# Performance work log

Hardware: AMD Instinct MI355X
Metric: run time of the kernel (lower is better)

The kernel has to match this reference:

```python
import jax, jax.numpy as jnp
import numpy as np

DIM = 512
DIM2 = 2 * DIM
HEADS = 8
HEAD_DIM = DIM2 // HEADS
NB = 4                      # BlockDiagonalLinear blocks
BLK = DIM2 // NB
KS = 4                      # causal conv kernel size
EPS = 1e-5


def setup_inputs() -> dict:
    key = jax.random.key(0)
    ks = jax.random.split(key, 32)
    r = lambda i, shape, s=0.02: jax.random.normal(ks[i], shape, dtype=jnp.float32) * s
    inp = {
        "x": jax.random.normal(ks[0], (2, 2048, DIM), dtype=jnp.float32),
        "ln_w": jnp.ones((DIM,), jnp.float32),
        "ln_b": jnp.zeros((DIM,), jnp.float32),
        "mlp1_w": r(1, (DIM, DIM2)), "mlp1_b": jnp.zeros((DIM2,), jnp.float32),
        "mlp2_w": r(2, (DIM, DIM2)), "mlp2_b": jnp.zeros((DIM2,), jnp.float32),
        "conv_w": r(3, (DIM2, DIM2, KS)), "conv_b": jnp.zeros((DIM2,), jnp.float32),
        "bq_w": r(4, (NB, BLK, BLK)), "bk_w": r(5, (NB, BLK, BLK)), "bv_w": r(6, (NB, BLK, BLK)),
        "wq_w": r(7, (DIM2, DIM2)), "wq_b": jnp.zeros((DIM2,), jnp.float32),
        "wk_w": r(8, (DIM2, DIM2)), "wk_b": jnp.zeros((DIM2,), jnp.float32),
        "wv_w": r(9, (DIM2, DIM2)), "wv_b": jnp.zeros((DIM2,), jnp.float32),
        "wi_w": r(10, (DIM2, HEADS)), "wi_b": jnp.zeros((HEADS,), jnp.float32),
        "wf_w": r(11, (DIM2, HEADS)), "wf_b": jnp.zeros((HEADS,), jnp.float32),
        "gn_w": jnp.ones((DIM2,), jnp.float32), "gn_b": jnp.zeros((DIM2,), jnp.float32),
        "skip": jnp.ones((DIM2,), jnp.float32),
        "fin_w": r(12, (DIM2, DIM)), "fin_b": jnp.zeros((DIM,), jnp.float32),
    }
    return inp


def _layernorm(x, w, b):
    mu = jnp.mean(x, -1, keepdims=True)
    var = jnp.var(x, -1, keepdims=True)
    return (x - mu) * jax.lax.rsqrt(var + EPS) * w + b


def _block_linear(x, w):  # x: [b,s,DIM2], w: [NB, BLK, BLK]
    b, s, _ = x.shape
    xg = x.reshape(b, s, NB, BLK)
    return jnp.einsum('bsgi,gio->bsgo', xg, w).reshape(b, s, DIM2)


def _mlstm_cell(q, k, v, wq_w, wq_b, wk_w, wk_b, wv_w, wv_b,
                wi_w, wi_b, wf_w, wf_b, gn_w, gn_b):
    b, s, _ = q.shape
    tau = DIM2 ** 0.5
    itilde = jnp.einsum('bsd,dh->bhs', q, wi_w) + wi_b[None, :, None]   # [b,h,s]
    ftilde = jnp.einsum('bsd,dh->bhs', k, wf_w) + wf_b[None, :, None]   # [b,h,s]
    # cumulative log forget gates; F_act[i,j] = cs[i] - cs[j] on lower triangle
    cs = jnp.cumsum(jax.nn.log_sigmoid(ftilde), axis=-1)                # [b,h,s]
    mask = jnp.tril(jnp.ones((s, s), bool))
    Dtilde = jnp.where(mask,
                       cs[..., :, None] - cs[..., None, :] + itilde[..., None, :],
                       -jnp.inf)                                        # [b,h,s,s]
    max_d = jnp.max(Dtilde, axis=-1, keepdims=True)
    D = jnp.exp(Dtilde - max_d)
    qh = (q @ wq_w + wq_b).reshape(b, s, HEADS, HEAD_DIM).transpose(0, 2, 1, 3)
    kh = (k @ wk_w + wk_b).reshape(b, s, HEADS, HEAD_DIM).transpose(0, 2, 1, 3)
    vh = (v @ wv_w + wv_b).reshape(b, s, HEADS, HEAD_DIM).transpose(0, 2, 1, 3)
    Ctilde = jnp.einsum('bhid,bhjd->bhij', qh, kh) * D / tau
    maxit = jnp.maximum(jnp.abs(Ctilde.sum(-1)), jnp.exp(-max_d[..., 0]))  # [b,h,s]
    H = jnp.einsum('bhij,bhjd->bhid', Ctilde, vh) / (maxit[..., None] + 1e-8)
    H = H.transpose(0, 2, 1, 3)                                          # [b,s,h,hd]
    # GroupNorm(heads, DIM2): per (b,s,head-group) normalization
    mu = jnp.mean(H, -1, keepdims=True)
    var = jnp.var(H, -1, keepdims=True)
    Hn = (H - mu) * jax.lax.rsqrt(var + EPS)
    Hn = Hn * gn_w.reshape(HEADS, HEAD_DIM) + gn_b.reshape(HEADS, HEAD_DIM)
    return Hn.reshape(b, s, DIM2)


def reference(x, ln_w, ln_b, mlp1_w, mlp1_b, mlp2_w, mlp2_b, conv_w, conv_b,
              bq_w, bk_w, bv_w, wq_w, wq_b, wk_w, wk_b, wv_w, wv_b,
              wi_w, wi_b, wf_w, wf_b, gn_w, gn_b, skip, fin_w, fin_b):
    inputs = _layernorm(x, ln_w, ln_b)
    a = inputs @ mlp1_w + mlp1_b                 # [b,s,DIM2]
    bgate = jax.nn.silu(inputs @ mlp2_w + mlp2_b)
    # causal conv1d (left pad KS-1)
    ac = a.transpose(0, 2, 1)                    # [b,DIM2,s]
    qk = jax.lax.conv_general_dilated(ac, conv_w, (1,), [(KS - 1, 0)],
                                      dimension_numbers=('NCH', 'OIH', 'NCH'))
    qk = (qk + conv_b[None, :, None]).transpose(0, 2, 1)
    qk = jax.nn.silu(qk)
    q = _block_linear(qk, bq_w)
    k = _block_linear(qk, bk_w)
    v = _block_linear(a, bv_w)
    out1 = _mlstm_cell(q, k, v, wq_w, wq_b, wk_w, wk_b, wv_w, wv_b,
                       wi_w, wi_b, wf_w, wf_b, gn_w, gn_b)
    out1 = out1 + skip * qk
    out1 = out1 * bgate
    out1 = out1 @ fin_w + fin_b
    return x + out1
```

## Files before the change

kernel.cpp:

```cpp
#include <hip/hip_runtime.h>
#include <hip/hip_bf16.h>
#include <cmath>

typedef __hip_bfloat16 bf16;
typedef __attribute__((ext_vector_type(8))) short short8;
typedef __attribute__((ext_vector_type(4))) float f32x4;

#define SEQ   2048
#define DIMX  512
#define DIM2X 1024
#define NHEADS 8
#define HDIM  128
#define EPSF  1e-5f
#define PADROWS 2051

__device__ __forceinline__ float b2f(bf16 v) { return __bfloat162float(v); }
__device__ __forceinline__ bf16 f2b(float f) { return __float2bfloat16(f); }
__device__ __forceinline__ unsigned short f2bu(float f) { bf16 t = __float2bfloat16(f); return *(unsigned short*)&t; }

__device__ __forceinline__ void gl16(const bf16* g, bf16* l) {
  __builtin_amdgcn_global_load_lds((const __attribute__((address_space(1))) void*)g,
                                   (__attribute__((address_space(3))) void*)l, 16, 0, 0);
}

__global__ void __launch_bounds__(256) k_layernorm(const float* __restrict__ x,
                                                   const float* __restrict__ w,
                                                   const float* __restrict__ b,
                                                   bf16* __restrict__ out) {
  int row  = blockIdx.x * 4 + (threadIdx.x >> 6);
  int lane = threadIdx.x & 63;
  const float* xr = x + (size_t)row * DIMX;
  float v[8]; float s = 0.f, sq = 0.f;
#pragma unroll
  for (int i = 0; i < 8; i++) {
    float f = xr[lane + i * 64];
    v[i] = f; s += f; sq += f * f;
  }
#pragma unroll
  for (int off = 32; off; off >>= 1) { s += __shfl_xor(s, off); sq += __shfl_xor(sq, off); }
  float mu  = s * (1.f / DIMX);
  float var = sq * (1.f / DIMX) - mu * mu;
  float rs  = rsqrtf(var + EPSF);
  bf16* o = out + (size_t)row * DIMX;
#pragma unroll
  for (int i = 0; i < 8; i++) {
    int c = lane + i * 64;
    o[c] = f2b((v[i] - mu) * rs * w[c] + b[c]);
  }
}

__global__ void __launch_bounds__(256) k_castT3(const float* __restrict__ W0,
                                                const float* __restrict__ W1,
                                                const float* __restrict__ W2,
                                                bf16* __restrict__ WT,
                                                int K, int N, int innerZ, int gW, int gT) {
  __shared__ float t[32][33];
  const int z = blockIdx.z;
  const int sel = z / innerZ, zz = z % innerZ;
  const float* W = (sel == 0 ? W0 : sel == 1 ? W1 : W2) + (size_t)zz * gW;
  bf16* T = WT + (size_t)(sel * innerZ + zz) * gT;
  const int k0 = blockIdx.y * 32, n0 = blockIdx.x * 32;
  const int r = threadIdx.x >> 5, c = threadIdx.x & 31;
#pragma unroll
  for (int i = 0; i < 4; i++)
    t[r + i * 8][c] = W[(size_t)(k0 + r + i * 8) * N + n0 + c];
  __syncthreads();
#pragma unroll
  for (int i = 0; i < 4; i++)
    T[(size_t)(n0 + r + i * 8) * K + k0 + c] = f2b(t[c][r + i * 8]);
}

__global__ void __launch_bounds__(256) k_convwT(const float* __restrict__ cw, bf16* __restrict__ wc) {
  int idx = blockIdx.x * 256 + threadIdx.x;
  int o = idx >> 12, z = idx & 4095, kk = z >> 10, i = z & 1023;
  wc[idx] = f2b(cw[(size_t)o * 4096 + i * 4 + kk]);
}

__global__ void __launch_bounds__(256) k_zeropad(bf16* __restrict__ p) {
  int idx = blockIdx.x * 256 + threadIdx.x;
  int b = idx / 3072, off = idx % 3072;
  p[(size_t)b * PADROWS * DIM2X + off] = f2b(0.f);
}

__device__ __forceinline__ void mgemm_body(const bf16* A, int lda, const bf16* WT,
                                           const float* bias, void* Cv, const float* xres,
                                           int ldc, int K, int ACT, int STORE, int APAD,
                                           size_t coff, int bm, int bn) {
  __shared__ __align__(16) bf16 smA[4][128 * 32];
  __shared__ __align__(16) bf16 smB[4][64 * 32];
  const int tid  = threadIdx.x;
  const int lane = tid & 63;
  const int w = tid >> 6, wy = w >> 1, wx = w & 1;
  const int col = lane & 15, quad = lane >> 4;

  const int r4 = tid >> 2, c8 = (tid & 3) * 8;
  int ra0 = bm + r4, ra1 = bm + 64 + r4;
  if (APAD) { ra0 += (ra0 >> 11) * 3 + 3; ra1 += (ra1 >> 11) * 3 + 3; }
  const bf16* gA0 = A + (size_t)ra0 * lda + c8;
  const bf16* gA1 = A + (size_t)ra1 * lda + c8;
  const bf16* gB0 = WT + (size_t)(bn + r4) * K + c8;

  f32x4 acc[4][2];
#pragma unroll
  for (int a = 0; a < 4; a++)
#pragma unroll
    for (int b = 0; b < 2; b++) acc[a][b] = (f32x4){0.f, 0.f, 0.f, 0.f};

  const int laoff = (wy * 64) * 32, lboff = (wx * 32) * 32;
  const int lsa = r4 * 32 + c8;
  const int nsteps = K >> 5;

#define GSTAGE(buf, k0s)                                                       \
  do {                                                                         \
    gl16(gA0 + (k0s), &smA[buf][lsa]);                                         \
    gl16(gA1 + (k0s), &smA[buf][64 * 32 + lsa]);                               \
    gl16(gB0 + (k0s), &smB[buf][lsa]);                                         \
  } while (0)

  GSTAGE(0, 0);
  if (nsteps > 1) GSTAGE(1, 32);
  for (int s = 0; s < nsteps; ++s) {
    if (s + 2 < nsteps) GSTAGE((s + 2) & 3, (s + 2) * 32);
    if (s + 2 < nsteps)      asm volatile("s_waitcnt vmcnt(6)" ::: "memory");
    else if (s + 1 < nsteps) asm volatile("s_waitcnt vmcnt(3)" ::: "memory");
    else                     asm volatile("s_waitcnt vmcnt(0)" ::: "memory");
    __builtin_amdgcn_s_barrier();
    asm volatile("" ::: "memory");
    const bf16* bA = smA[s & 3];
    const bf16* bB = smB[s & 3];
    short8 af[4], bfr[2];
#pragma unroll
    for (int mt = 0; mt < 4; mt++)
      af[mt] = *(const short8*)&bA[laoff + (mt * 16 + col) * 32 + quad * 8];
#pragma unroll
    for (int nt = 0; nt < 2; nt++)
      bfr[nt] = *(const short8*)&bB[lboff + (nt * 16 + col) * 32 + quad * 8];
#pragma unroll
    for (int mt = 0; mt < 4; mt++)
#pragma unroll
      for (int nt = 0; nt < 2; nt++)
        acc[mt][nt] = __builtin_amdgcn_mfma_f32_16x16x32_bf16(af[mt], bfr[nt], acc[mt][nt], 0, 0, 0);
  }
#undef GSTAGE

#pragma unroll
  for (int mt = 0; mt < 4; mt++) {
#pragma unroll
    for (int nt = 0; nt < 2; nt++) {
      const int n = bn + wx * 32 + nt * 16 + col;
      const int mrow0 = bm + wy * 64 + mt * 16 + quad * 4;
      float bs = bias ? bias[n] : 0.f;
      if (STORE == 1) {
        bf16* C = (bf16*)Cv + coff;
        ushort4 pk;
        pk.x = f2bu(acc[mt][nt][0] + bs); pk.y = f2bu(acc[mt][nt][1] + bs);
        pk.z = f2bu(acc[mt][nt][2] + bs); pk.w = f2bu(acc[mt][nt][3] + bs);
        *(ushort4*)(C + (size_t)n * 4096 + mrow0) = pk;
      } else if (STORE == 2) {
        float* O = (float*)Cv + coff;
#pragma unroll
        for (int r = 0; r < 4; r++) {
          size_t gi = (size_t)(mrow0 + r) * ldc + n;
          O[gi] = acc[mt][nt][r] + bs + xres[gi];
        }
      } else if (STORE == 3) {
        bf16* C = (bf16*)Cv;
        const int pr = (mrow0 >> 11) * 3 + 3;
#pragma unroll
        for (int r = 0; r < 4; r++)
          C[(size_t)(mrow0 + pr + r) * ldc + n] = f2b(acc[mt][nt][r] + bs);
      } else {
        bf16* C = (bf16*)Cv + coff;
#pragma unroll
        for (int r = 0; r < 4; r++) {
          float v = acc[mt][nt][r] + bs;
          if (ACT == 1) v = v / (1.f + expf(-v));
          C[(size_t)(mrow0 + r) * ldc + n] = f2b(v);
        }
      }
    }
  }
}

__device__ __forceinline__ int xcd_work_id() {
  const int nx = gridDim.x, ny = gridDim.y;
  const int d = blockIdx.x + nx * (blockIdx.y + ny * blockIdx.z);
  const int q = (nx * ny * (int)gridDim.z) >> 3;
  return (d & 7) * q + (d >> 3);
}

template <int ACT, int STORE, int APAD>
__global__ void __launch_bounds__(256) k_mgemm(const bf16* __restrict__ A, int lda,
                                               const bf16* __restrict__ WT,
                                               const float* __restrict__ bias,
                                               void* __restrict__ Cv,
                                               const float* __restrict__ xres,
                                               int ldc, int K,
                                               int gA, int gW, int gC) {
  const int wk = xcd_work_id();
  const int nx = gridDim.x, ny = gridDim.y;
  const int wx = wk % nx, rest = wk / nx;
  const int wy = rest % ny, g = rest / ny;
  mgemm_body(A + (size_t)g * gA, lda, WT + (size_t)g * gW, bias, Cv, xres,
             ldc, K, ACT, STORE, APAD, (size_t)g * gC, wy * 128, wx * 64);
}

__global__ void __launch_bounds__(256) k_mgemmB(const bf16* A0, const bf16* A1, const bf16* A2,
                                                const bf16* W0, const bf16* W1, const bf16* W2,
                                                const float* b0, const float* b1, const float* b2,
                                                void* C0, void* C1, void* C2,
                                                int lda, int ldc, int K, int zPer,
                                                int gA, int gW, int gC,
                                                int actm, int storem, int apadm) {
  const int wk = xcd_work_id();
  const int nx = gridDim.x, ny = gridDim.y;
  const int wx = wk % nx, rest = wk / nx;
  const int wy = rest % ny, z = rest / ny;
  const int sel = z / zPer, zz = z % zPer;
  const bf16* A = (sel == 0 ? A0 : sel == 1 ? A1 : A2) + (size_t)zz * gA;
  const bf16* W = (sel == 0 ? W0 : sel == 1 ? W1 : W2) + (size_t)zz * gW;
  const float* bias = sel == 0 ? b0 : sel == 1 ? b1 : b2;
  void* Cv = sel == 0 ? C0 : sel == 1 ? C1 : C2;
  mgemm_body(A, lda, W, bias, Cv, nullptr, ldc, K,
             (actm >> sel) & 1, (storem >> (4 * sel)) & 15, (apadm >> sel) & 1,
             (size_t)zz * gC, wy * 128, wx * 64);
}

__global__ void __launch_bounds__(256) k_gates(const bf16* __restrict__ q, const bf16* __restrict__ kk,
                                               const float* __restrict__ wi, const float* __restrict__ wib,
                                               const float* __restrict__ wf, const float* __restrict__ wfb,
                                               float* __restrict__ it, float* __restrict__ ft) {
  int gid  = blockIdx.x * 4 + (threadIdx.x >> 6);
  int lane = threadIdx.x & 63;
  int which = gid >> 12;
  int m = gid & 4095;
  const bf16* row = (which ? kk : q) + (size_t)m * DIM2X;
  const float* w = which ? wf : wi;
  float s[8] = {0, 0, 0, 0, 0, 0, 0, 0};
  for (int d = lane; d < DIM2X; d += 64) {
    float xv = b2f(row[d]);
    const float4* wp = (const float4*)(w + d * 8);
    float4 w0 = wp[0], w1 = wp[1];
    s[0] += xv * w0.x; s[1] += xv * w0.y; s[2] += xv * w0.z; s[3] += xv * w0.w;
    s[4] += xv * w1.x; s[5] += xv * w1.y; s[6] += xv * w1.z; s[7] += xv * w1.w;
  }
#pragma unroll
  for (int off = 32; off; off >>= 1) {
#pragma unroll
    for (int h = 0; h < 8; h++) s[h] += __shfl_xor(s[h], off);
  }
  if (lane == 0) {
    int b_ = m >> 11, tt = m & 2047;
    const float* wb = which ? wfb : wib;
    float* dst = which ? ft : it;
#pragma unroll
    for (int h = 0; h < 8; h++)
      dst[((size_t)(b_ * NHEADS + h)) * SEQ + tt] = s[h] + wb[h];
  }
}

__global__ void __launch_bounds__(256) k_scan(const float* __restrict__ it, const float* __restrict__ ft,
                                              float* __restrict__ cs, float* __restrict__ md) {
  const int bh = blockIdx.x;
  const int t  = threadIdx.x;
  const float* fr = ft + (size_t)bh * SEQ;
  const float* ir = it + (size_t)bh * SEQ;
  float* csr = cs + (size_t)bh * SEQ;
  float* mdr = md + (size_t)bh * SEQ;
  __shared__ float tmp[256];
  float loc[8]; float run = 0.f;
#pragma unroll
  for (int j = 0; j < 8; j++) {
    float xv = fr[t * 8 + j];
    float ls = fminf(xv, 0.f) - log1pf(expf(-fabsf(xv)));
    run += ls; loc[j] = run;
  }
  tmp[t] = run;
  __syncthreads();
  for (int off = 1; off < 256; off <<= 1) {
    float add = (t >= off) ? tmp[t - off] : 0.f;
    __syncthreads();
    tmp[t] += add;
    __syncthreads();
  }
  float exc = (t == 0) ? 0.f : tmp[t - 1];
  float csv[8];
#pragma unroll
  for (int j = 0; j < 8; j++) { csv[j] = loc[j] + exc; csr[t * 8 + j] = csv[j]; }
  __syncthreads();
  float rmax = -INFINITY; float gm[8];
#pragma unroll
  for (int j = 0; j < 8; j++) {
    float gv = ir[t * 8 + j] - csv[j];
    rmax = fmaxf(rmax, gv); gm[j] = rmax;
  }
  tmp[t] = rmax;
  __syncthreads();
  for (int off = 1; off < 256; off <<= 1) {
    float other = (t >= off) ? tmp[t - off] : -INFINITY;
    __syncthreads();
    tmp[t] = fmaxf(tmp[t], other);
    __syncthreads();
  }
  float emax = (t == 0) ? -INFINITY : tmp[t - 1];
#pragma unroll
  for (int j = 0; j < 8; j++) mdr[t * 8 + j] = csv[j] + fmaxf(gm[j], emax);
}

__global__ void __launch_bounds__(256) k_attn_mfma(const bf16* __restrict__ qh,
                                                   const bf16* __restrict__ kh,
                                                   const bf16* __restrict__ vt,
                                                   const float* __restrict__ cs,
                                                   const float* __restrict__ md,
                                                   const float* __restrict__ itl,
                                                   bf16* __restrict__ Hout) {
  const int bh = blockIdx.y, b_ = bh >> 3, h = bh & 7;
  const int pr = blockIdx.x;
  const int tid = threadIdx.x;
  const int w = tid >> 6;
  const int lane = tid & 63;
  const int col = lane & 15, quad = lane >> 4;
  const float L2E = 1.44269504f;

  __shared__ __align__(16) bf16 smK[4 * 4096];
  __shared__ __align__(16) bf16 smV[4 * 4096];
  __shared__ __align__(16) bf16 Sc[4][16][40];

  const size_t baseQK = ((size_t)b_ * SEQ) * DIM2X + (size_t)h * HDIM;
  const size_t vtb = (size_t)(h * HDIM) * 4096 + (size_t)b_ * SEQ;
  const float* csp = cs + (size_t)bh * SEQ;
  const float* mdp = md + (size_t)bh * SEQ;
  const float* itp = itl + (size_t)bh * SEQ;

  const int kj = tid >> 4, kq = tid & 15;
  const bf16* gKs = kh + baseQK + (size_t)kj * DIM2X + ((kq ^ (kj & 7)) * 8);
  const int vn = tid >> 2, vq = tid & 3;
  const bf16* gVs = vt + vtb + (size_t)vn * 4096 + ((vq ^ ((vn >> 1) & 3)) * 8);

#define STAGE(buf, j0s)                                                        \
  do {                                                                         \
    bf16* dK = &smK[(buf) * 4096 + tid * 8];                                   \
    gl16(gKs + (size_t)(j0s) * DIM2X, dK);                                     \
    gl16(gKs + (size_t)((j0s) + 16) * DIM2X, dK + 2048);                       \
    bf16* dV = &smV[(buf) * 4096 + tid * 8];                                   \
    gl16(gVs + (j0s), dV);                                                     \
    gl16(gVs + (j0s) + (size_t)64 * 4096, dV + 2048);                          \
  } while (0)

  for (int ph = 0; ph < 2; ++ph) {
    const int tile = ph ? (31 - pr) : pr;
    const int i0 = tile * 64;
    const int i0w = i0 + w * 16;
    const int iwmax = i0w + 15;

    short8 qf[4];
#pragma unroll
    for (int kc = 0; kc < 4; kc++)
      qf[kc] = *(const short8*)(qh + baseQK + (size_t)(i0w + col) * DIM2X + kc * 32 + quad * 8);

    float cs_i[4], md_i[4];
#pragma unroll
    for (int r = 0; r < 4; r++) {
      int i = i0w + quad * 4 + r;
      cs_i[r] = csp[i] * L2E; md_i[r] = mdp[i] * L2E;
    }

    f32x4 accpv[8];
#pragma unroll
    for (int nb = 0; nb < 8; nb++) accpv[nb] = (f32x4){0.f, 0.f, 0.f, 0.f};
    float rs[4] = {0.f, 0.f, 0.f, 0.f};

    const int trips = 2 * tile + 2;
    STAGE(0, 0);
    STAGE(1, 32);
    for (int t = 0; t < trips; ++t) {
      const int cur = t & 3;
      const int j0p = t * 32;
      if (t + 2 < trips) STAGE((t + 2) & 3, j0p + 64);
      if (t + 2 < trips)      asm volatile("s_waitcnt vmcnt(8)" ::: "memory");
      else if (t + 1 < trips) asm volatile("s_waitcnt vmcnt(4)" ::: "memory");
      else                    asm volatile("s_waitcnt vmcnt(0)" ::: "memory");
      __builtin_amdgcn_s_barrier();
      asm volatile("" ::: "memory");
      if (j0p <= iwmax) {
        float g0 = (itp[j0p + col] - csp[j0p + col]) * L2E;
        float g1 = (itp[j0p + 16 + col] - csp[j0p + 16 + col]) * L2E;
        const bool jt1 = (j0p + 16 <= iwmax);
#pragma unroll
        for (int jt = 0; jt < 2; jt++) {
          const int j0 = j0p + jt * 16;
          float sv[4] = {0.f, 0.f, 0.f, 0.f};
          if (jt == 0 || jt1) {
            const int jj = jt * 16 + col;
            f32x4 aq = (f32x4){0.f, 0.f, 0.f, 0.f};
#pragma unroll
            for (int kc = 0; kc < 4; kc++) {
              short8 bk = *(const short8*)&smK[cur * 4096 + jj * 128 + ((((kc << 2) | quad) ^ (jj & 7)) << 3)];
              aq = __builtin_amdgcn_mfma_f32_16x16x32_bf16(qf[kc], bk, aq, 0, 0, 0);
            }
            const int j = j0 + col;
            const float gj = jt ? g1 : g0;
#pragma unroll
            for (int r = 0; r < 4; r++) {
              const int i = i0w + quad * 4 + r;
              float s = (j <= i) ? exp2f(cs_i[r] + gj - md_i[r] - 5.f) * aq[r] : 0.f;
              sv[r] = s; rs[r] += s;
            }
          }
#pragma unroll
          for (int r = 0; r < 4; r++) Sc[w][quad * 4 + r][jt * 16 + col] = f2b(sv[r]);
        }
        asm volatile("s_waitcnt lgkmcnt(0)" ::: "memory");
        __builtin_amdgcn_sched_barrier(0);
        short8 af = *(const short8*)(&Sc[w][col][quad * 8]);
#pragma unroll
        for (int nb = 0; nb < 8; nb++) {
          const int rn = nb * 16 + col;
          short8 bv = *(const short8*)&smV[cur * 4096 + rn * 32 + ((quad ^ ((rn >> 1) & 3)) << 3)];
          accpv[nb] = __builtin_amdgcn_mfma_f32_16x16x32_bf16(af, bv, accpv[nb], 0, 0, 0);
        }
      }
    }
    __syncthreads();

#pragma unroll
    for (int r = 0; r < 4; r++) {
      float v = rs[r];
      v += __shfl_xor(v, 1); v += __shfl_xor(v, 2);
      v += __shfl_xor(v, 4); v += __shfl_xor(v, 8);
      rs[r] = v;
    }
    float inv[4];
#pragma unroll
    for (int r = 0; r < 4; r++) {
      float maxit = fmaxf(fabsf(rs[r]), exp2f(fminf(-md_i[r], 43.f)));
      inv[r] = 1.f / (maxit + 1e-8f);
    }
#pragma unroll
    for (int nb = 0; nb < 8; nb++)
#pragma unroll
      for (int r = 0; r < 4; r++)
        Hout[baseQK + (size_t)(i0w + quad * 4 + r) * DIM2X + nb * 16 + col] = f2b(accpv[nb][r] * inv[r]);
  }
#undef STAGE
}

__global__ void __launch_bounds__(256) k_gnorm(const bf16* __restrict__ H, const bf16* __restrict__ qk,
                                               const bf16* __restrict__ bg,
                                               const float* __restrict__ gw, const float* __restrict__ gb,
                                               const float* __restrict__ skip, bf16* __restrict__ pre) {
  int gid  = blockIdx.x * 4 + (threadIdx.x >> 6);
  int lane = threadIdx.x & 63;
  int m = gid >> 3, h = gid & 7;
  const bf16* Hr = H + (size_t)m * DIM2X + (size_t)h * HDIM;
  float v0 = b2f(Hr[lane]), v1 = b2f(Hr[lane + 64]);
  float s = v0 + v1, sq = v0 * v0 + v1 * v1;
#pragma unroll
  for (int off = 32; off; off >>= 1) { s += __shfl_xor(s, off); sq += __shfl_xor(sq, off); }
  float mu  = s * (1.f / 128.f);
  float var = sq * (1.f / 128.f) - mu * mu;
  float rs  = rsqrtf(var + EPSF);
#pragma unroll
  for (int e = 0; e < 2; e++) {
    int c = lane + e * 64;
    int col = h * HDIM + c;
    float v = e ? v1 : v0;
    float hn = (v - mu) * rs * gw[col] + gb[col];
    size_t gidx = (size_t)m * DIM2X + col;
    pre[gidx] = f2b((hn + skip[col] * b2f(qk[gidx])) * b2f(bg[gidx]));
  }
}

extern "C" void kernel_launch(void* const* d_in, const int* in_sizes, int n_in,
                              void* d_out, int out_size, void* d_ws, size_t ws_size,
                              hipStream_t stream) {
  const float* x     = (const float*)d_in[0];
  const float* ln_w  = (const float*)d_in[1];
  const float* ln_b  = (const float*)d_in[2];
  const float* mlp1w = (const float*)d_in[3];
  const float* mlp1b = (const float*)d_in[4];
  const float* mlp2w = (const float*)d_in[5];
  const float* mlp2b = (const float*)d_in[6];
  const float* convw = (const float*)d_in[7];
  const float* convb = (const float*)d_in[8];
  const float* bqw   = (const float*)d_in[9];
  const float* bkw   = (const float*)d_in[10];
  const float* bvw   = (const float*)d_in[11];
  const float* wqw   = (const float*)d_in[12];
  const float* wqb   = (const float*)d_in[13];
  const float* wkw   = (const float*)d_in[14];
  const float* wkb   = (const float*)d_in[15];
  const float* wvw   = (const float*)d_in[16];
  const float* wvb   = (const float*)d_in[17];
  const float* wiw   = (const float*)d_in[18];
  const float* wib   = (const float*)d_in[19];
  const float* wfw   = (const float*)d_in[20];
  const float* wfb   = (const float*)d_in[21];
  const float* gnw   = (const float*)d_in[22];
  const float* gnb   = (const float*)d_in[23];
  const float* skip  = (const float*)d_in[24];
  const float* finw  = (const float*)d_in[25];
  const float* finb  = (const float*)d_in[26];
  float* out = (float*)d_out;

  float* GA  = (float*)d_ws;
  float* ITb = GA;
  float* FTb = GA + 32768;
  float* CSb = GA + 65536;
  float* MDb = GA + 98304;
  const size_t SLOT = 4u * 1024u * 1024u;
  bf16* S0 = (bf16*)((char*)d_ws + (1 << 20));
  bf16* S1 = S0 + SLOT;
  bf16* S2 = S1 + SLOT;
  bf16* S3 = S2 + SLOT;
  bf16* S4 = S3 + SLOT;
  bf16* S5 = S4 + SLOT;
  bf16* S6 = S5 + SLOT;
  bf16 *LN = S0, *BG = S2, *QKb = S3, *Qb = S4, *Kb = S5, *Vb = S6;
  bf16 *QH = S0, *KH = S1, *VT = S4, *Hb = S5, *PRE = S6;
  bf16* WTb   = S6 + SLOT;
  bf16* mlp1T = WTb;
  bf16* mlp2T = WTb + 524288;
  bf16* convT = WTb + 1048576;
  bf16* bqT   = WTb + 5242880;
  bf16* bkT   = bqT + 262144;
  bf16* bvT   = bkT + 262144;
  bf16* wqT   = bvT + 262144;
  bf16* wkT   = wqT + 1048576;
  bf16* wvT   = wkT + 1048576;
  bf16* finT  = wvT + 1048576;
  bf16* APD   = finT + 524288;

  k_castT3<<<dim3(32, 16, 2), 256, 0, stream>>>(mlp1w, mlp2w, mlp2w, mlp1T, DIMX, DIM2X, 1, 0, 524288);
  k_castT3<<<dim3(32, 32, 3), 256, 0, stream>>>(wqw, wkw, wvw, wqT, DIM2X, DIM2X, 1, 0, 1048576);
  k_castT3<<<dim3(8, 8, 12), 256, 0, stream>>>(bqw, bkw, bvw, bqT, 256, 256, 4, 65536, 65536);
  k_castT3<<<dim3(16, 32, 1), 256, 0, stream>>>(finw, finw, finw, finT, DIM2X, DIMX, 1, 0, 524288);
  k_convwT<<<16384, 256, 0, stream>>>(convw, convT);
  k_zeropad<<<24, 256, 0, stream>>>(APD);

  k_layernorm<<<1024, 256, 0, stream>>>(x, ln_w, ln_b, LN);
  k_mgemmB<<<dim3(16, 32, 2), 256, 0, stream>>>(LN, LN, LN, mlp1T, mlp2T, mlp2T,
                                                mlp1b, mlp2b, mlp2b, APD, BG, BG,
                                                DIMX, DIM2X, DIMX, 1, 0, 0, 0,
                                                 0b10,  3 | (0 << 4),  0);
  k_mgemm<1, 0, 0><<<dim3(16, 16, 2), 256, 0, stream>>>(APD, DIM2X, convT, convb, QKb, nullptr,
                                                        DIM2X, 4096, PADROWS * DIM2X, 0, SEQ * DIM2X);
  k_mgemmB<<<dim3(4, 32, 12), 256, 0, stream>>>(QKb, QKb, APD, bqT, bkT, bvT,
                                                nullptr, nullptr, nullptr, Qb, Kb, Vb,
                                                DIM2X, DIM2X, 256, 4, 256, 65536, 256,
                                                 0,  0,  0b100);
  k_gates<<<2048, 256, 0, stream>>>(Qb, Kb, wiw, wib, wfw, wfb, ITb, FTb);
  k_scan<<<16, 256, 0, stream>>>(ITb, FTb, CSb, MDb);
  k_mgemmB<<<dim3(16, 32, 3), 256, 0, stream>>>(Qb, Kb, Vb, wqT, wkT, wvT,
                                                wqb, wkb, wvb, QH, KH, VT,
                                                DIM2X, DIM2X, DIM2X, 1, 0, 0, 0,
                                                 0,  0 | (0 << 4) | (1 << 8),  0);
  k_attn_mfma<<<dim3(16, 16), 256, 0, stream>>>(QH, KH, VT, CSb, MDb, ITb, Hb);
  k_gnorm<<<8192, 256, 0, stream>>>(Hb, QKb, BG, gnw, gnb, skip, PRE);
  k_mgemm<0, 2, 0><<<dim3(8, 32), 256, 0, stream>>>(PRE, DIM2X, finT, finb, out, x, DIMX, DIM2X, 0, 0, 0);
}
```

Measured before the change: 460.5 us.

## Fuse group-norm/skip/gate epilogue into attention kernel and split tile pairs into blocks

The per-head group norm, skip connection and output gate move into the attention kernel's epilogue, using in-register accumulators with shuffle reductions across the 128 head columns. This removes the separate gnorm kernel and the bf16 H buffer round-trip. The attention grid is also doubled so each block processes one query tile rather than a paired short/long tile, with ordering alternated by batch. This raises parallelism but may worsen causal load balance.

```diff
diff --git a/kernel.cpp b/kernel.cpp
--- a/kernel.cpp
+++ b/kernel.cpp
@@ -313,13 +313,22 @@
                                                    const float* __restrict__ cs,
                                                    const float* __restrict__ md,
                                                    const float* __restrict__ itl,
-                                                   bf16* __restrict__ Hout) {
+                                                   const bf16* __restrict__ qk,
+                                                   const bf16* __restrict__ bg,
+                                                   const float* __restrict__ gw,
+                                                   const float* __restrict__ gb,
+                                                   const float* __restrict__ skip,
+                                                   bf16* __restrict__ pre) {
   const int bh = blockIdx.y, b_ = bh >> 3, h = bh & 7;
-  const int pr = blockIdx.x;
+  const int bx = blockIdx.x;
+  const int tile = ((blockIdx.y >> 3) & 1) ? bx : 31 - bx;
+  const int i0 = tile * 64;
   const int tid = threadIdx.x;
   const int w = tid >> 6;
   const int lane = tid & 63;
   const int col = lane & 15, quad = lane >> 4;
+  const int i0w = i0 + w * 16;
+  const int iwmax = i0w + 15;
   const float L2E = 1.44269504f;
 
   __shared__ __align__(16) bf16 smK[4 * 4096];
@@ -332,10 +341,29 @@
   const float* mdp = md + (size_t)bh * SEQ;
   const float* itp = itl + (size_t)bh * SEQ;
 
+  short8 qf[4];
+#pragma unroll
+  for (int kc = 0; kc < 4; kc++)
+    qf[kc] = *(const short8*)(qh + baseQK + (size_t)(i0w + col) * DIM2X + kc * 32 + quad * 8);
+
+  float cs_i[4], md_i[4];
+#pragma unroll
+  for (int r = 0; r < 4; r++) {
+    int i = i0w + quad * 4 + r;
+    cs_i[r] = csp[i] * L2E; md_i[r] = mdp[i] * L2E;
+  }
+
+  f32x4 accpv[8];
+#pragma unroll
+  for (int nb = 0; nb < 8; nb++) accpv[nb] = (f32x4){0.f, 0.f, 0.f, 0.f};
+  float rs[4] = {0.f, 0.f, 0.f, 0.f};
+
   const int kj = tid >> 4, kq = tid & 15;
   const bf16* gKs = kh + baseQK + (size_t)kj * DIM2X + ((kq ^ (kj & 7)) * 8);
   const int vn = tid >> 2, vq = tid & 3;
   const bf16* gVs = vt + vtb + (size_t)vn * 4096 + ((vq ^ ((vn >> 1) & 3)) * 8);
+
+  const int trips = 2 * tile + 2;
 
 #define STAGE(buf, j0s)                                                        \
   do {                                                                         \
@@ -347,127 +375,101 @@
     gl16(gVs + (j0s) + (size_t)64 * 4096, dV + 2048);                          \
   } while (0)
 
-  for (int ph = 0; ph < 2; ++ph) {
-    const int tile = ph ? (31 - pr) : pr;
-    const int i0 = tile * 64;
-    const int i0w = i0 + w * 16;
-    const int iwmax = i0w + 15;
-
-    short8 qf[4];
-#pragma unroll
-    for (int kc = 0; kc < 4; kc++)
-      qf[kc] = *(const short8*)(qh + baseQK + (size_t)(i0w + col) * DIM2X + kc * 32 + quad * 8);
-
-    float cs_i[4], md_i[4];
-#pragma unroll
-    for (int r = 0; r < 4; r++) {
-      int i = i0w + quad * 4 + r;
-      cs_i[r] = csp[i] * L2E; md_i[r] = mdp[i] * L2E;
-    }
-
-    f32x4 accpv[8];
-#pragma unroll
-    for (int nb = 0; nb < 8; nb++) accpv[nb] = (f32x4){0.f, 0.f, 0.f, 0.f};
-    float rs[4] = {0.f, 0.f, 0.f, 0.f};
-
-    const int trips = 2 * tile + 2;
-    STAGE(0, 0);
-    STAGE(1, 32);
-    for (int t = 0; t < trips; ++t) {
-      const int cur = t & 3;
-      const int j0p = t * 32;
-      if (t + 2 < trips) STAGE((t + 2) & 3, j0p + 64);
-      if (t + 2 < trips)      asm volatile("s_waitcnt vmcnt(8)" ::: "memory");
-      else if (t + 1 < trips) asm volatile("s_waitcnt vmcnt(4)" ::: "memory");
-      else                    asm volatile("s_waitcnt vmcnt(0)" ::: "memory");
-      __builtin_amdgcn_s_barrier();
-      asm volatile("" ::: "memory");
-      if (j0p <= iwmax) {
-        float g0 = (itp[j0p + col] - csp[j0p + col]) * L2E;
-        float g1 = (itp[j0p + 16 + col] - csp[j0p + 16 + col]) * L2E;
-        const bool jt1 = (j0p + 16 <= iwmax);
-#pragma unroll
-        for (int jt = 0; jt < 2; jt++) {
-          const int j0 = j0p + jt * 16;
-          float sv[4] = {0.f, 0.f, 0.f, 0.f};
-          if (jt == 0 || jt1) {
-            const int jj = jt * 16 + col;
-            f32x4 aq = (f32x4){0.f, 0.f, 0.f, 0.f};
-#pragma unroll
-            for (int kc = 0; kc < 4; kc++) {
-              short8 bk = *(const short8*)&smK[cur * 4096 + jj * 128 + ((((kc << 2) | quad) ^ (jj & 7)) << 3)];
-              aq = __builtin_amdgcn_mfma_f32_16x16x32_bf16(qf[kc], bk, aq, 0, 0, 0);
-            }
-            const int j = j0 + col;
-            const float gj = jt ? g1 : g0;
-#pragma unroll
-            for (int r = 0; r < 4; r++) {
-              const int i = i0w + quad * 4 + r;
-              float s = (j <= i) ? exp2f(cs_i[r] + gj - md_i[r] - 5.f) * aq[r] : 0.f;
-              sv[r] = s; rs[r] += s;
-            }
+  STAGE(0, 0);
+  STAGE(1, 32);
+  for (int t = 0; t < trips; ++t) {
+    const int cur = t & 3;
+    const int j0p = t * 32;
+    if (t + 2 < trips) STAGE((t + 2) & 3, j0p + 64);
+    if (t + 2 < trips)      asm volatile("s_waitcnt vmcnt(8)" ::: "memory");
+    else if (t + 1 < trips) asm volatile("s_waitcnt vmcnt(4)" ::: "memory");
+    else                    asm volatile("s_waitcnt vmcnt(0)" ::: "memory");
+    __builtin_amdgcn_s_barrier();
+    asm volatile("" ::: "memory");
+    if (j0p <= iwmax) {
+      float g0 = (itp[j0p + col] - csp[j0p + col]) * L2E;
+      float g1 = (itp[j0p + 16 + col] - csp[j0p + 16 + col]) * L2E;
+      const bool jt1 = (j0p + 16 <= iwmax);
+#pragma unroll
+      for (int jt = 0; jt < 2; jt++) {
+        const int j0 = j0p + jt * 16;
+        float sv[4] = {0.f, 0.f, 0.f, 0.f};
+        if (jt == 0 || jt1) {
+          const int jj = jt * 16 + col;
+          f32x4 aq = (f32x4){0.f, 0.f, 0.f, 0.f};
+#pragma unroll
+          for (int kc = 0; kc < 4; kc++) {
+            short8 bk = *(const short8*)&smK[cur * 4096 + jj * 128 + ((((kc << 2) | quad) ^ (jj & 7)) << 3)];
+            aq = __builtin_amdgcn_mfma_f32_16x16x32_bf16(qf[kc], bk, aq, 0, 0, 0);
           }
-#pragma unroll
-          for (int r = 0; r < 4; r++) Sc[w][quad * 4 + r][jt * 16 + col] = f2b(sv[r]);
+          const int j = j0 + col;
+          const float gj = jt ? g1 : g0;
+#pragma unroll
+          for (int r = 0; r < 4; r++) {
+            const int i = i0w + quad * 4 + r;
+            float s = (j <= i) ? exp2f(cs_i[r] + gj - md_i[r] - 5.f) * aq[r] : 0.f;
+            sv[r] = s; rs[r] += s;
+          }
         }
-        asm volatile("s_waitcnt lgkmcnt(0)" ::: "memory");
-        __builtin_amdgcn_sched_barrier(0);
-        short8 af = *(const short8*)(&Sc[w][col][quad * 8]);
-#pragma unroll
-        for (int nb = 0; nb < 8; nb++) {
-          const int rn = nb * 16 + col;
-          short8 bv = *(const short8*)&smV[cur * 4096 + rn * 32 + ((quad ^ ((rn >> 1) & 3)) << 3)];
-          accpv[nb] = __builtin_amdgcn_mfma_f32_16x16x32_bf16(af, bv, accpv[nb], 0, 0, 0);
-        }
+#pragma unroll
+        for (int r = 0; r < 4; r++) Sc[w][quad * 4 + r][jt * 16 + col] = f2b(sv[r]);
+      }
+      asm volatile("s_waitcnt lgkmcnt(0)" ::: "memory");
+      __builtin_amdgcn_sched_barrier(0);
+      short8 af = *(const short8*)(&Sc[w][col][quad * 8]);
+#pragma unroll
+      for (int nb = 0; nb < 8; nb++) {
+        const int rn = nb * 16 + col;
+        short8 bv = *(const short8*)&smV[cur * 4096 + rn * 32 + ((quad ^ ((rn >> 1) & 3)) << 3)];
+        accpv[nb] = __builtin_amdgcn_mfma_f32_16x16x32_bf16(af, bv, accpv[nb], 0, 0, 0);
       }
     }
-    __syncthreads();
-
-#pragma unroll
-    for (int r = 0; r < 4; r++) {
-      float v = rs[r];
-      v += __shfl_xor(v, 1); v += __shfl_xor(v, 2);
-      v += __shfl_xor(v, 4); v += __shfl_xor(v, 8);
-      rs[r] = v;
+  }
+#undef STAGE
+
+#pragma unroll
+  for (int r = 0; r < 4; r++) {
+    float v = rs[r];
+    v += __shfl_xor(v, 1); v += __shfl_xor(v, 2);
+    v += __shfl_xor(v, 4); v += __shfl_xor(v, 8);
+    rs[r] = v;
+  }
+  float inv[4];
+#pragma unroll
+  for (int r = 0; r < 4; r++) {
+    float maxit = fmaxf(fabsf(rs[r]), exp2f(fminf(-md_i[r], 43.f)));
+    inv[r] = 1.f / (maxit + 1e-8f);
+  }
+  float gwv[8], gbv[8], skv[8];
+#pragma unroll
+  for (int nb = 0; nb < 8; nb++) {
+    int c = h * HDIM + nb * 16 + col;
+    gwv[nb] = gw[c]; gbv[nb] = gb[c]; skv[nb] = skip[c];
+  }
+#pragma unroll
+  for (int r = 0; r < 4; r++) {
+    const int row = i0w + quad * 4 + r;
+    float s1 = 0.f, s2 = 0.f;
+#pragma unroll
+    for (int nb = 0; nb < 8; nb++) {
+      float v = accpv[nb][r] * inv[r];
+      s1 += v; s2 += v * v;
     }
-    float inv[4];
-#pragma unroll
-    for (int r = 0; r < 4; r++) {
-      float maxit = fmaxf(fabsf(rs[r]), exp2f(fminf(-md_i[r], 43.f)));
-      inv[r] = 1.f / (maxit + 1e-8f);
+    s1 += __shfl_xor(s1, 1); s2 += __shfl_xor(s2, 1);
+    s1 += __shfl_xor(s1, 2); s2 += __shfl_xor(s2, 2);
+    s1 += __shfl_xor(s1, 4); s2 += __shfl_xor(s2, 4);
+    s1 += __shfl_xor(s1, 8); s2 += __shfl_xor(s2, 8);
+    float mu  = s1 * (1.f / 128.f);
+    float var = s2 * (1.f / 128.f) - mu * mu;
+    float rsg = rsqrtf(var + EPSF);
+    const size_t rbase = baseQK + (size_t)row * DIM2X;
+#pragma unroll
+    for (int nb = 0; nb < 8; nb++) {
+      float hv = accpv[nb][r] * inv[r];
+      float hn = (hv - mu) * rsg * gwv[nb] + gbv[nb];
+      size_t gi = rbase + nb * 16 + col;
+      pre[gi] = f2b((hn + skv[nb] * b2f(qk[gi])) * b2f(bg[gi]));
     }
-#pragma unroll
-    for (int nb = 0; nb < 8; nb++)
-#pragma unroll
-      for (int r = 0; r < 4; r++)
-        Hout[baseQK + (size_t)(i0w + quad * 4 + r) * DIM2X + nb * 16 + col] = f2b(accpv[nb][r] * inv[r]);
-  }
-#undef STAGE
-}
-
-__global__ void __launch_bounds__(256) k_gnorm(const bf16* __restrict__ H, const bf16* __restrict__ qk,
-                                               const bf16* __restrict__ bg,
-                                               const float* __restrict__ gw, const float* __restrict__ gb,
-                                               const float* __restrict__ skip, bf16* __restrict__ pre) {
-  int gid  = blockIdx.x * 4 + (threadIdx.x >> 6);
-  int lane = threadIdx.x & 63;
-  int m = gid >> 3, h = gid & 7;
-  const bf16* Hr = H + (size_t)m * DIM2X + (size_t)h * HDIM;
-  float v0 = b2f(Hr[lane]), v1 = b2f(Hr[lane + 64]);
-  float s = v0 + v1, sq = v0 * v0 + v1 * v1;
-#pragma unroll
-  for (int off = 32; off; off >>= 1) { s += __shfl_xor(s, off); sq += __shfl_xor(sq, off); }
-  float mu  = s * (1.f / 128.f);
-  float var = sq * (1.f / 128.f) - mu * mu;
-  float rs  = rsqrtf(var + EPSF);
-#pragma unroll
-  for (int e = 0; e < 2; e++) {
-    int c = lane + e * 64;
-    int col = h * HDIM + c;
-    float v = e ? v1 : v0;
-    float hn = (v - mu) * rs * gw[col] + gb[col];
-    size_t gidx = (size_t)m * DIM2X + col;
-    pre[gidx] = f2b((hn + skip[col] * b2f(qk[gidx])) * b2f(bg[gidx]));
   }
 }
 
@@ -517,7 +519,7 @@
   bf16* S5 = S4 + SLOT;
   bf16* S6 = S5 + SLOT;
   bf16 *LN = S0, *BG = S2, *QKb = S3, *Qb = S4, *Kb = S5, *Vb = S6;
-  bf16 *QH = S0, *KH = S1, *VT = S4, *Hb = S5, *PRE = S6;
+  bf16 *QH = S0, *KH = S1, *VT = S4, *PRE = S6;
   bf16* WTb   = S6 + SLOT;
   bf16* mlp1T = WTb;
   bf16* mlp2T = WTb + 524288;
@@ -555,7 +557,7 @@
                                                 wqb, wkb, wvb, QH, KH, VT,
                                                 DIM2X, DIM2X, DIM2X, 1, 0, 0, 0,
                                                  0,  0 | (0 << 4) | (1 << 8),  0);
-  k_attn_mfma<<<dim3(16, 16), 256, 0, stream>>>(QH, KH, VT, CSb, MDb, ITb, Hb);
-  k_gnorm<<<8192, 256, 0, stream>>>(Hb, QKb, BG, gnw, gnb, skip, PRE);
+  k_attn_mfma<<<dim3(32, 16), 256, 0, stream>>>(QH, KH, VT, CSb, MDb, ITb,
+                                                QKb, BG, gnw, gnb, skip, PRE);
   k_mgemm<0, 2, 0><<<dim3(8, 32), 256, 0, stream>>>(PRE, DIM2X, finT, finb, out, x, DIMX, DIM2X, 0, 0, 0);
 }
```

Result: faster. 444.9 us (-3.4%).
